# Optimization experiments

Measured on AMD Instinct MI355X. Metric: run time of the kernel, lower is better.

## Reference

```python
import jax, jax.numpy as jnp
import numpy as np

N_NODES = 50000
N_EDGES = 200000
D = 128
LN_EPS = 1e-5


def _layer_norm(x, g, b):
    mu = jnp.mean(x, axis=-1, keepdims=True)
    var = jnp.mean(jnp.square(x - mu), axis=-1, keepdims=True)
    return (x - mu) * jax.lax.rsqrt(var + LN_EPS) * g + b


def _mlp(x, W1, b1, W2, b2, W3, b3, g, beta):
    # 2 hidden ReLU layers + linear output + LayerNorm (MeshGraphNets style)
    h = jax.nn.relu(x @ W1 + b1)
    h = jax.nn.relu(h @ W2 + b2)
    h = h @ W3 + b3
    return _layer_norm(h, g, beta)


def setup_inputs() -> dict:
    key = jax.random.key(0)
    ks = jax.random.split(key, 12)
    d = {}
    d["node_features"] = jax.random.normal(ks[0], (N_NODES, D), dtype=jnp.float32)
    d["edge_features"] = jax.random.normal(ks[1], (N_EDGES, D), dtype=jnp.float32)
    d["senders"] = jax.random.randint(ks[2], (N_EDGES,), 0, N_NODES, dtype=jnp.int32)
    d["receivers"] = jax.random.randint(ks[3], (N_EDGES,), 0, N_NODES, dtype=jnp.int32)
    def lin(k, fan_in, fan_out):
        return jax.random.normal(k, (fan_in, fan_out), dtype=jnp.float32) / np.sqrt(fan_in)
    # edge MLP: [3D] -> D -> D -> D
    d["We1"] = lin(ks[4], 3 * D, D); d["be1"] = jnp.zeros((D,), jnp.float32)
    d["We2"] = lin(ks[5], D, D);     d["be2"] = jnp.zeros((D,), jnp.float32)
    d["We3"] = lin(ks[6], D, D);     d["be3"] = jnp.zeros((D,), jnp.float32)
    d["ge"] = jnp.ones((D,), jnp.float32); d["bege"] = jnp.zeros((D,), jnp.float32)
    # node MLP: [2D] -> D -> D -> D
    d["Wn1"] = lin(ks[7], 2 * D, D); d["bn1"] = jnp.zeros((D,), jnp.float32)
    d["Wn2"] = lin(ks[8], D, D);     d["bn2"] = jnp.zeros((D,), jnp.float32)
    d["Wn3"] = lin(ks[9], D, D);     d["bn3"] = jnp.zeros((D,), jnp.float32)
    d["gn"] = jnp.ones((D,), jnp.float32); d["begn"] = jnp.zeros((D,), jnp.float32)
    return d


def reference(node_features, edge_features, senders, receivers,
              We1, be1, We2, be2, We3, be3, ge, bege,
              Wn1, bn1, Wn2, bn2, Wn3, bn3, gn, begn):
    num_nodes = node_features.shape[0]
    # --- edge update: gather sender/receiver feats, concat, edge MLP ---
    edge_in = jnp.concatenate(
        [node_features[senders], node_features[receivers], edge_features], axis=-1)  # [E, 3D]
    new_edge = _mlp(edge_in, We1, be1, We2, be2, We3, be3, ge, bege)  # [E, D]
    # --- node update: scatter-sum aggregate, concat, node MLP ---
    agg = jax.ops.segment_sum(new_edge, receivers, num_segments=num_nodes)  # [N, D]
    node_in = jnp.concatenate([node_features, agg], axis=-1)  # [N, 2D]
    new_node = _mlp(node_in, Wn1, bn1, Wn2, bn2, Wn3, bn3, gn, begn)
    # --- residuals ---
    new_node = new_node + node_features
    new_edge = new_edge + edge_features
    return new_node, new_edge
```

## Files before the change

kernel.cpp:

```cpp
#include <hip/hip_runtime.h>

#define NNODES 50000
#define NEDGES 200000
#define DD 128
#define LN_EPS 1e-5f
#define NTH 256

typedef __attribute__((ext_vector_type(8))) short bf16x8;
typedef __attribute__((ext_vector_type(4))) float f32x4;

template<int N> struct ic { static constexpr int value = N; };

__device__ __forceinline__ unsigned short bf_rne(float f) {
    union { float f; unsigned u; } v; v.f = f;
    return (unsigned short)((v.u + 0x7fffu + ((v.u >> 16) & 1u)) >> 16);
}

__device__ __forceinline__ void gload_lds16(const void* g, void* l) {
    __builtin_amdgcn_global_load_lds(
        (const __attribute__((address_space(1))) void*)g,
        (__attribute__((address_space(3))) void*)l, 16, 0, 0);
}

__global__ void build_wimg(const float* __restrict__ We1, const float* __restrict__ We2,
                           const float* __restrict__ We3, const float* __restrict__ Wn1,
                           const float* __restrict__ Wn2, const float* __restrict__ Wn3,
                           char* __restrict__ img_e, char* __restrict__ img_n) {
    int tid = blockIdx.x * NTH + threadIdx.x;
    const float* W; char* dst; int q;
    if      (tid <  6144) { W = We1; dst = img_e;             q = tid;         }
    else if (tid <  8192) { W = We2; dst = img_e + 12 * 8192; q = tid - 6144;  }
    else if (tid < 10240) { W = We3; dst = img_e + 16 * 8192; q = tid - 8192;  }
    else if (tid < 14336) { W = Wn1; dst = img_n;             q = tid - 10240; }
    else if (tid < 16384) { W = Wn2; dst = img_n + 8 * 8192;  q = tid - 14336; }
    else if (tid < 18432) { W = Wn3; dst = img_n + 12 * 8192; q = tid - 16384; }
    else return;
    int c = q >> 9, rem = q & 511, n = rem >> 2, g = rem & 3;
    int S = ((g + (n >> 2)) & 3) ^ (n & 3);
    int k0 = c * 32 + g * 8;
    unsigned short o[8];
    #pragma unroll
    for (int e = 0; e < 8; ++e)
        o[e] = bf_rne(W[(size_t)(k0 + e) * DD + n]);
    uint4 val;
    val.x = (unsigned)o[0] | ((unsigned)o[1] << 16);
    val.y = (unsigned)o[2] | ((unsigned)o[3] << 16);
    val.z = (unsigned)o[4] | ((unsigned)o[5] << 16);
    val.w = (unsigned)o[6] | ((unsigned)o[7] << 16);
    *(uint4*)(dst + (size_t)c * 8192 + n * 64 + S * 16) = val;
}

__global__ void csr_histo(const int* __restrict__ recv, int* __restrict__ cnt) {
    int e = blockIdx.x * NTH + threadIdx.x;
    if (e < NEDGES) atomicAdd(&cnt[recv[e]], 1);
}

__global__ __launch_bounds__(1024)
void csr_scan(const int* __restrict__ cnt, int* __restrict__ off, int* __restrict__ cursor) {
    __shared__ int part[1024];
    const int t = threadIdx.x;
    const int CH = (NNODES + 1023) / 1024;
    const int base = t * CH;
    int s = 0;
    for (int i = 0; i < CH; ++i) {
        int idx = base + i;
        if (idx < NNODES) s += cnt[idx];
    }
    part[t] = s;
    __syncthreads();
    for (int d = 1; d < 1024; d <<= 1) {
        int v = (t >= d) ? part[t - d] : 0;
        __syncthreads();
        part[t] += v;
        __syncthreads();
    }
    int run = (t == 0) ? 0 : part[t - 1];
    for (int i = 0; i < CH; ++i) {
        int idx = base + i;
        if (idx < NNODES) {
            off[idx] = run; cursor[idx] = run;
            run += cnt[idx];
        }
    }
    if (t == 1023) off[NNODES] = NEDGES;
}

__global__ void csr_fill(const int* __restrict__ recv, int* __restrict__ cursor,
                         int* __restrict__ elist) {
    int e = blockIdx.x * NTH + threadIdx.x;
    if (e < NEDGES) {
        int p = atomicAdd(&cursor[recv[e]], 1);
        elist[p] = e;
    }
}

__global__ __launch_bounds__(NTH)
void aggregate(const float* __restrict__ oute, const float* __restrict__ edgef,
               const int* __restrict__ off, const int* __restrict__ elist,
               float* __restrict__ agg) {
    const int n = blockIdx.x * 4 + (threadIdx.x >> 6);
    const int l = threadIdx.x & 63;
    if (n >= NNODES) return;
    const int j0 = off[n], j1 = off[n + 1];
    float ax = 0.f, ay = 0.f, bx = 0.f, by = 0.f;
    int j = j0;
    for (; j + 1 < j1; j += 2) {
        const int e0 = elist[j], e1 = elist[j + 1];
        const float2 o0 = ((const float2*)(oute  + (size_t)e0 * DD))[l];
        const float2 f0 = ((const float2*)(edgef + (size_t)e0 * DD))[l];
        const float2 o1 = ((const float2*)(oute  + (size_t)e1 * DD))[l];
        const float2 f1 = ((const float2*)(edgef + (size_t)e1 * DD))[l];
        ax += o0.x - f0.x; ay += o0.y - f0.y;
        bx += o1.x - f1.x; by += o1.y - f1.y;
    }
    if (j < j1) {
        const int e = elist[j];
        const float2 o  = ((const float2*)(oute  + (size_t)e * DD))[l];
        const float2 ef = ((const float2*)(edgef + (size_t)e * DD))[l];
        ax += o.x - ef.x; ay += o.y - ef.y;
    }
    float2 r; r.x = ax + bx; r.y = ay + by;
    ((float2*)(agg + (size_t)n * DD))[l] = r;
}

template<int MODE>
__global__ __launch_bounds__(NTH, 3)
void mgn_mfma(const float* __restrict__ nodef, const float* __restrict__ edgef,
              const int* __restrict__ senders, const int* __restrict__ receivers,
              const char* __restrict__ img,
              const float* __restrict__ b1, const float* __restrict__ b2,
              const float* __restrict__ b3,
              const float* __restrict__ gamma, const float* __restrict__ beta,
              const float* __restrict__ agg, float* __restrict__ outp)
{
    __shared__ char Wbuf[4 * 8192];
    __shared__ char Hb[16384];

    const int t  = threadIdx.x;
    const int w  = t >> 6;
    const int l  = t & 63;
    const int lr = l & 15;
    const int g  = l >> 4;
    const int m_local = w * 16 + lr;
    const int row0 = blockIdx.x * 64;
    const int gm = row0 + m_local;
    constexpr int NROWS = (MODE == 0) ? NEDGES : NNODES;
    constexpr int NK1   = (MODE == 0) ? 12 : 8;
    constexpr int NCH   = NK1 + 8;
    const int gmc = gm < NROWS ? gm : NROWS - 1;
    const unsigned swz = (unsigned)(lr & 7) << 4;
    const int aoff = lr * 64 + ((((g + (lr >> 2)) & 3) ^ (lr & 3)) << 4);

    int srow = 0, rrow = 0;
    if (MODE == 0) { srow = senders[gmc]; rrow = receivers[gmc]; }

    f32x4 acc[8];
    const f32x4 fzero = {0.f, 0.f, 0.f, 0.f};
    #pragma unroll
    for (int nt = 0; nt < 8; ++nt) acc[nt] = fzero;

    f32x4 barr[3][2];

    auto stageW = [&](int c) {
        const char* src = img + (size_t)c * 8192 + w * 1024 + l * 16;
        char* dstl = Wbuf + (c & 3) * 8192 + w * 1024;
        gload_lds16(src, dstl);
        gload_lds16(src + 4096, dstl + 4096);
    };

    auto loadBG = [&](int c, f32x4* dst) {
        const float* base;
        if (MODE == 0) {
            base = (c < 4) ? nodef + (size_t)srow * DD
                 : (c < 8) ? nodef + (size_t)rrow * DD
                           : edgef + (size_t)gmc * DD;
        } else {
            base = (c < 4) ? nodef + (size_t)gmc * DD
                           : agg   + (size_t)gmc * DD;
        }
        const float* p = base + (c & 3) * 32 + g * 8;
        dst[0] = *(const f32x4*)p;
        dst[1] = *(const f32x4*)(p + 4);
    };

    auto cvtB = [&](const f32x4* br) {
        bf16x8 r;
        #pragma unroll
        for (int i = 0; i < 4; ++i) r[i]     = (short)bf_rne(br[0][i]);
        #pragma unroll
        for (int i = 0; i < 4; ++i) r[4 + i] = (short)bf_rne(br[1][i]);
        return r;
    };

    auto loadBH = [&](int ks) {
        const char* p = &Hb[(ks >> 1) * 8192] + m_local * 128
                      + ((unsigned)((ks & 1) * 64 + g * 16) ^ swz);
        return *(const bf16x8*)p;
    };

    auto epiH = [&](const float* bias) {
        #pragma unroll
        for (int nt = 0; nt < 8; ++nt) {
            f32x4 bv = *(const f32x4*)(bias + nt * 16 + g * 4);
            unsigned short h[4];
            #pragma unroll
            for (int r = 0; r < 4; ++r)
                h[r] = bf_rne(fmaxf(acc[nt][r] + bv[r], 0.f));
            char* p = &Hb[(nt >> 2) * 8192] + m_local * 128
                    + ((unsigned)(((nt & 3) * 2 + (g >> 1)) * 16) ^ swz) + (g & 1) * 8;
            unsigned lo = (unsigned)h[0] | ((unsigned)h[1] << 16);
            unsigned hi = (unsigned)h[2] | ((unsigned)h[3] << 16);
            *(unsigned long long*)p = (unsigned long long)lo | ((unsigned long long)hi << 32);
            acc[nt] = fzero;
        }
    };

    auto compute = [&](auto cc) {
        constexpr int c = decltype(cc)::value;
        const char* bp = Wbuf + (c & 3) * 8192 + aoff;
        bf16x8 a[8];
        #pragma unroll
        for (int nt = 0; nt < 8; ++nt)
            a[nt] = *(const bf16x8*)(bp + nt * 1024);
        bf16x8 b;
        if constexpr (c < NK1) b = cvtB(barr[c % 3]);
        else                   b = loadBH((c - NK1) & 3);
        #pragma unroll
        for (int nt = 0; nt < 8; ++nt)
            acc[nt] = __builtin_amdgcn_mfma_f32_16x16x32_bf16(a[nt], b, acc[nt], 0, 0, 0);
    };

#define PITER(C, VM)                                                        \
    {                                                                       \
        if constexpr ((C) + 2 < NCH) stageW((C) + 2);                       \
        __builtin_amdgcn_sched_barrier(0);                                  \
        if constexpr ((C) + 2 < NK1) loadBG((C) + 2, barr[((C) + 2) % 3]);  \
        __builtin_amdgcn_sched_barrier(0);                                  \
        asm volatile("s_waitcnt vmcnt(" #VM ")" ::: "memory");              \
        __builtin_amdgcn_sched_barrier(0);                                  \
        __builtin_amdgcn_s_barrier();                                       \
        __builtin_amdgcn_sched_barrier(0);                                  \
        compute(ic<(C)>{});                                                 \
    }

    stageW(0);
    __builtin_amdgcn_sched_barrier(0);
    loadBG(0, barr[0]);
    __builtin_amdgcn_sched_barrier(0);
    stageW(1);
    __builtin_amdgcn_sched_barrier(0);
    loadBG(1, barr[1]);
    __builtin_amdgcn_sched_barrier(0);

    if constexpr (MODE == 0) {
        PITER(0, 8)  PITER(1, 8)  PITER(2, 8)  PITER(3, 8)  PITER(4, 8)
        PITER(5, 8)  PITER(6, 8)  PITER(7, 8)  PITER(8, 8)  PITER(9, 8)
        PITER(10, 6) PITER(11, 4)
        epiH(b1);
        PITER(12, 4) PITER(13, 4) PITER(14, 4) PITER(15, 4)
        epiH(b2);
        PITER(16, 4) PITER(17, 4) PITER(18, 2) PITER(19, 0)
    } else {
        PITER(0, 8)  PITER(1, 8)  PITER(2, 8)  PITER(3, 8)  PITER(4, 8)
        PITER(5, 8)  PITER(6, 6)  PITER(7, 4)
        epiH(b1);
        PITER(8, 4)  PITER(9, 4)  PITER(10, 4) PITER(11, 4)
        epiH(b2);
        PITER(12, 4) PITER(13, 4) PITER(14, 2) PITER(15, 0)
    }
#undef PITER

    float vsum = 0.f, vsq = 0.f;
    #pragma unroll
    for (int nt = 0; nt < 8; ++nt) {
        f32x4 bv = *(const f32x4*)(b3 + nt * 16 + g * 4);
        #pragma unroll
        for (int r = 0; r < 4; ++r) {
            float v = acc[nt][r] + bv[r];
            acc[nt][r] = v;
            vsum += v; vsq += v * v;
        }
    }
    vsum += __shfl_xor(vsum, 16); vsum += __shfl_xor(vsum, 32);
    vsq  += __shfl_xor(vsq, 16);  vsq  += __shfl_xor(vsq, 32);
    const float mu = vsum * (1.f / DD);
    const float rs = rsqrtf(vsq * (1.f / DD) - mu * mu + LN_EPS);

    if (gm < NROWS) {
        const float* resid = ((MODE == 0) ? edgef : nodef) + (size_t)gm * DD;
        #pragma unroll
        for (int nt = 0; nt < 8; ++nt) {
            const int n0 = nt * 16 + g * 4;
            f32x4 gv = *(const f32x4*)(gamma + n0);
            f32x4 bv = *(const f32x4*)(beta + n0);
            f32x4 rv = *(const f32x4*)(resid + n0);
            f32x4 o;
            #pragma unroll
            for (int r = 0; r < 4; ++r)
                o[r] = (acc[nt][r] - mu) * rs * gv[r] + bv[r] + rv[r];
            *(f32x4*)(outp + (size_t)gm * DD + n0) = o;
        }
    }
}

extern "C" void kernel_launch(void* const* d_in, const int* in_sizes, int n_in,
                              void* d_out, int out_size, void* d_ws, size_t ws_size,
                              hipStream_t stream) {
    const float* nodef = (const float*)d_in[0];
    const float* edgef = (const float*)d_in[1];
    const int* senders   = (const int*)d_in[2];
    const int* receivers = (const int*)d_in[3];
    const float* We1 = (const float*)d_in[4],  *be1 = (const float*)d_in[5];
    const float* We2 = (const float*)d_in[6],  *be2 = (const float*)d_in[7];
    const float* We3 = (const float*)d_in[8],  *be3 = (const float*)d_in[9];
    const float* ge  = (const float*)d_in[10], *bege = (const float*)d_in[11];
    const float* Wn1 = (const float*)d_in[12], *bn1 = (const float*)d_in[13];
    const float* Wn2 = (const float*)d_in[14], *bn2 = (const float*)d_in[15];
    const float* Wn3 = (const float*)d_in[16], *bn3 = (const float*)d_in[17];
    const float* gn  = (const float*)d_in[18], *begn = (const float*)d_in[19];

    float* out_node = (float*)d_out;
    float* out_edge = (float*)d_out + (size_t)NNODES * DD;

    char* ws = (char*)d_ws;
    size_t o = 0;
    float* agg  = (float*)(ws + o); o += (size_t)NNODES * DD * 4;
    char* img_e = ws + o;           o += 20 * 8192;
    char* img_n = ws + o;           o += 16 * 8192;
    int* cnt    = (int*)(ws + o);   o += NNODES * 4;
    int* cursor = (int*)(ws + o);   o += NNODES * 4;
    int* off    = (int*)(ws + o);   o += (NNODES + 4) * 4;
    int* elist  = (int*)(ws + o);   o += NEDGES * 4;

    hipMemsetAsync(cnt, 0, NNODES * 4, stream);
    build_wimg<<<72, NTH, 0, stream>>>(We1, We2, We3, Wn1, Wn2, Wn3, img_e, img_n);

    const int egrid = (NEDGES + NTH - 1) / NTH;
    csr_histo<<<egrid, NTH, 0, stream>>>(receivers, cnt);
    csr_scan<<<1, 1024, 0, stream>>>(cnt, off, cursor);
    csr_fill<<<egrid, NTH, 0, stream>>>(receivers, cursor, elist);

    mgn_mfma<0><<<dim3((NEDGES + 63) / 64), dim3(NTH), 0, stream>>>(
        nodef, edgef, senders, receivers, img_e,
        be1, be2, be3, ge, bege, agg, out_edge);

    aggregate<<<(NNODES + 3) / 4, NTH, 0, stream>>>(out_edge, edgef, off, elist, agg);

    mgn_mfma<1><<<dim3((NNODES + 63) / 64), dim3(NTH), 0, stream>>>(
        nodef, edgef, senders, receivers, img_n,
        bn1, bn2, bn3, gn, begn, agg, out_node);
}
```

Baseline: 324.3 us.

## Switch fused MLP kernel to 32x32x16 MFMA tiles with 128-row blocks

The fused MLP kernel moves from 16x16x32 bf16 MFMA to 32x32x16 MFMA, so each wave now covers 32 rows and a block covers 128 rows. The weight image layout and LDS swizzles are rebuilt to match the new operand fragments. Weight staging goes from a 4-slot to a 5-slot ring with a prefetch distance of 3 chunks. The hidden-activation buffer doubles and launch bounds drop to 2 blocks per CU. The aim is higher MFMA throughput and more weight reuse per LDS load, at the cost of more registers and LDS and lower occupancy.

Result: no change. 329.2 us (+1.5%).

```diff
diff --git a/kernel.cpp b/kernel.cpp
--- a/kernel.cpp
+++ b/kernel.cpp
@@ -8,6 +8,7 @@
 
 typedef __attribute__((ext_vector_type(8))) short bf16x8;
 typedef __attribute__((ext_vector_type(4))) float f32x4;
+typedef __attribute__((ext_vector_type(16))) float f32x16;
 
 template<int N> struct ic { static constexpr int value = N; };
 
@@ -35,9 +36,11 @@
     else if (tid < 16384) { W = Wn2; dst = img_n + 8 * 8192;  q = tid - 14336; }
     else if (tid < 18432) { W = Wn3; dst = img_n + 12 * 8192; q = tid - 16384; }
     else return;
-    int c = q >> 9, rem = q & 511, n = rem >> 2, g = rem & 3;
-    int S = ((g + (n >> 2)) & 3) ^ (n & 3);
-    int k0 = c * 32 + g * 8;
+    int c = q >> 9, rem = q & 511;
+    int ntile = rem >> 7, r2 = rem & 127, n32 = r2 >> 2, ks = r2 & 3;
+    int n = ntile * 32 + n32;
+    int sx = (n32 + (n32 >> 2)) & 3;
+    int k0 = c * 32 + ks * 8;
     unsigned short o[8];
     #pragma unroll
     for (int e = 0; e < 8; ++e)
@@ -47,7 +50,7 @@
     val.y = (unsigned)o[2] | ((unsigned)o[3] << 16);
     val.z = (unsigned)o[4] | ((unsigned)o[5] << 16);
     val.w = (unsigned)o[6] | ((unsigned)o[7] << 16);
-    *(uint4*)(dst + (size_t)c * 8192 + n * 64 + S * 16) = val;
+    *(uint4*)(dst + (size_t)c * 8192 + ntile * 2048 + n32 * 64 + ((ks ^ sx) << 4)) = val;
 }
 
 __global__ void csr_histo(const int* __restrict__ recv, int* __restrict__ cnt) {
@@ -124,7 +127,7 @@
 }
 
 template<int MODE>
-__global__ __launch_bounds__(NTH, 3)
+__global__ __launch_bounds__(NTH, 2)
 void mgn_mfma(const float* __restrict__ nodef, const float* __restrict__ edgef,
               const int* __restrict__ senders, const int* __restrict__ receivers,
               const char* __restrict__ img,
@@ -133,37 +136,37 @@
               const float* __restrict__ gamma, const float* __restrict__ beta,
               const float* __restrict__ agg, float* __restrict__ outp)
 {
-    __shared__ char Wbuf[4 * 8192];
-    __shared__ char Hb[16384];
+    __shared__ char Wbuf[5 * 8192];
+    __shared__ char Hb[4 * 8192];
 
     const int t  = threadIdx.x;
     const int w  = t >> 6;
     const int l  = t & 63;
-    const int lr = l & 15;
-    const int g  = l >> 4;
-    const int m_local = w * 16 + lr;
-    const int row0 = blockIdx.x * 64;
-    const int gm = row0 + m_local;
+    const int ln = l & 31;
+    const int hi = l >> 5;
+    const int row0 = blockIdx.x * 128;
+    const int gm = row0 + w * 32 + ln;
     constexpr int NROWS = (MODE == 0) ? NEDGES : NNODES;
     constexpr int NK1   = (MODE == 0) ? 12 : 8;
     constexpr int NCH   = NK1 + 8;
     const int gmc = gm < NROWS ? gm : NROWS - 1;
-    const unsigned swz = (unsigned)(lr & 7) << 4;
-    const int aoff = lr * 64 + ((((g + (lr >> 2)) & 3) ^ (lr & 3)) << 4);
+    const int sxA = (ln + (ln >> 2)) & 3;
+    const int sxH = ln & 15;
 
     int srow = 0, rrow = 0;
     if (MODE == 0) { srow = senders[gmc]; rrow = receivers[gmc]; }
 
-    f32x4 acc[8];
-    const f32x4 fzero = {0.f, 0.f, 0.f, 0.f};
+    const f32x16 fz = {0.f,0.f,0.f,0.f,0.f,0.f,0.f,0.f,
+                       0.f,0.f,0.f,0.f,0.f,0.f,0.f,0.f};
+    f32x16 acc[4];
     #pragma unroll
-    for (int nt = 0; nt < 8; ++nt) acc[nt] = fzero;
-
-    f32x4 barr[3][2];
+    for (int nt = 0; nt < 4; ++nt) acc[nt] = fz;
+
+    f32x4 barr[3][4];
 
     auto stageW = [&](int c) {
-        const char* src = img + (size_t)c * 8192 + w * 1024 + l * 16;
-        char* dstl = Wbuf + (c & 3) * 8192 + w * 1024;
+        const char* src = img + (size_t)c * 8192 + t * 16;
+        char* dstl = Wbuf + (c % 5) * 8192 + t * 16;
         gload_lds16(src, dstl);
         gload_lds16(src + 4096, dstl + 4096);
     };
@@ -178,9 +181,11 @@
             base = (c < 4) ? nodef + (size_t)gmc * DD
                            : agg   + (size_t)gmc * DD;
         }
-        const float* p = base + (c & 3) * 32 + g * 8;
+        const float* p = base + (c & 3) * 32 + hi * 8;
         dst[0] = *(const f32x4*)p;
         dst[1] = *(const f32x4*)(p + 4);
+        dst[2] = *(const f32x4*)(p + 16);
+        dst[3] = *(const f32x4*)(p + 20);
     };
 
     auto cvtB = [&](const f32x4* br) {
@@ -192,47 +197,53 @@
         return r;
     };
 
-    auto loadBH = [&](int ks) {
-        const char* p = &Hb[(ks >> 1) * 8192] + m_local * 128
-                      + ((unsigned)((ks & 1) * 64 + g * 16) ^ swz);
+    auto loadBH = [&](int ks, int kh) {
+        const char* p = Hb + w * 8192 + ln * 256
+                      + (((ks * 4 + kh * 2 + hi) ^ sxH) << 4);
         return *(const bf16x8*)p;
     };
 
     auto epiH = [&](const float* bias) {
         #pragma unroll
-        for (int nt = 0; nt < 8; ++nt) {
-            f32x4 bv = *(const f32x4*)(bias + nt * 16 + g * 4);
-            unsigned short h[4];
+        for (int nt = 0; nt < 4; ++nt) {
             #pragma unroll
-            for (int r = 0; r < 4; ++r)
-                h[r] = bf_rne(fmaxf(acc[nt][r] + bv[r], 0.f));
-            char* p = &Hb[(nt >> 2) * 8192] + m_local * 128
-                    + ((unsigned)(((nt & 3) * 2 + (g >> 1)) * 16) ^ swz) + (g & 1) * 8;
-            unsigned lo = (unsigned)h[0] | ((unsigned)h[1] << 16);
-            unsigned hi = (unsigned)h[2] | ((unsigned)h[3] << 16);
-            *(unsigned long long*)p = (unsigned long long)lo | ((unsigned long long)hi << 32);
-            acc[nt] = fzero;
+            for (int rq = 0; rq < 4; ++rq) {
+                f32x4 bv = *(const f32x4*)(bias + nt * 32 + rq * 8 + hi * 4);
+                unsigned short h[4];
+                #pragma unroll
+                for (int j = 0; j < 4; ++j)
+                    h[j] = bf_rne(fmaxf(acc[nt][rq * 4 + j] + bv[j], 0.f));
+                char* p = Hb + w * 8192 + ln * 256
+                        + (((nt * 4 + rq) ^ sxH) << 4) + hi * 8;
+                unsigned lo = (unsigned)h[0] | ((unsigned)h[1] << 16);
+                unsigned hx = (unsigned)h[2] | ((unsigned)h[3] << 16);
+                *(unsigned long long*)p =
+                    (unsigned long long)lo | ((unsigned long long)hx << 32);
+            }
+            acc[nt] = fz;
         }
     };
 
     auto compute = [&](auto cc) {
         constexpr int c = decltype(cc)::value;
-        const char* bp = Wbuf + (c & 3) * 8192 + aoff;
-        bf16x8 a[8];
-        #pragma unroll
-        for (int nt = 0; nt < 8; ++nt)
-            a[nt] = *(const bf16x8*)(bp + nt * 1024);
-        bf16x8 b;
-        if constexpr (c < NK1) b = cvtB(barr[c % 3]);
-        else                   b = loadBH((c - NK1) & 3);
-        #pragma unroll
-        for (int nt = 0; nt < 8; ++nt)
-            acc[nt] = __builtin_amdgcn_mfma_f32_16x16x32_bf16(a[nt], b, acc[nt], 0, 0, 0);
+        const char* bp = Wbuf + (c % 5) * 8192 + ln * 64;
+        #pragma unroll
+        for (int kh = 0; kh < 2; ++kh) {
+            bf16x8 b;
+            if constexpr (c < NK1) b = cvtB(&barr[c % 3][kh * 2]);
+            else                   b = loadBH((c - NK1) & 3, kh);
+            #pragma unroll
+            for (int nt = 0; nt < 4; ++nt) {
+                bf16x8 a = *(const bf16x8*)(bp + nt * 2048
+                            + (((kh * 2 + hi) ^ sxA) << 4));
+                acc[nt] = __builtin_amdgcn_mfma_f32_32x32x16_bf16(a, b, acc[nt], 0, 0, 0);
+            }
+        }
     };
 
 #define PITER(C, VM)                                                        \
     {                                                                       \
-        if constexpr ((C) + 2 < NCH) stageW((C) + 2);                       \
+        if constexpr ((C) + 3 < NCH) stageW((C) + 3);                       \
         __builtin_amdgcn_sched_barrier(0);                                  \
         if constexpr ((C) + 2 < NK1) loadBG((C) + 2, barr[((C) + 2) % 3]);  \
         __builtin_amdgcn_sched_barrier(0);                                  \
@@ -251,54 +262,62 @@
     __builtin_amdgcn_sched_barrier(0);
     loadBG(1, barr[1]);
     __builtin_amdgcn_sched_barrier(0);
+    stageW(2);
+    __builtin_amdgcn_sched_barrier(0);
 
     if constexpr (MODE == 0) {
-        PITER(0, 8)  PITER(1, 8)  PITER(2, 8)  PITER(3, 8)  PITER(4, 8)
-        PITER(5, 8)  PITER(6, 8)  PITER(7, 8)  PITER(8, 8)  PITER(9, 8)
-        PITER(10, 6) PITER(11, 4)
+        PITER(0, 18)  PITER(1, 18)  PITER(2, 18)  PITER(3, 22)  PITER(4, 22)
+        PITER(5, 22)  PITER(6, 22)  PITER(7, 22)  PITER(8, 22)  PITER(9, 22)
+        PITER(10, 18) PITER(11, 14)
         epiH(b1);
-        PITER(12, 4) PITER(13, 4) PITER(14, 4) PITER(15, 4)
+        PITER(12, 10) PITER(13, 6)  PITER(14, 6)  PITER(15, 6)
         epiH(b2);
-        PITER(16, 4) PITER(17, 4) PITER(18, 2) PITER(19, 0)
+        PITER(16, 6)  PITER(17, 4)  PITER(18, 2)  PITER(19, 0)
     } else {
-        PITER(0, 8)  PITER(1, 8)  PITER(2, 8)  PITER(3, 8)  PITER(4, 8)
-        PITER(5, 8)  PITER(6, 6)  PITER(7, 4)
+        PITER(0, 18)  PITER(1, 18)  PITER(2, 18)  PITER(3, 22)  PITER(4, 22)
+        PITER(5, 22)  PITER(6, 18)  PITER(7, 14)
         epiH(b1);
-        PITER(8, 4)  PITER(9, 4)  PITER(10, 4) PITER(11, 4)
+        PITER(8, 10)  PITER(9, 6)   PITER(10, 6)  PITER(11, 6)
         epiH(b2);
-        PITER(12, 4) PITER(13, 4) PITER(14, 2) PITER(15, 0)
+        PITER(12, 6)  PITER(13, 4)  PITER(14, 2)  PITER(15, 0)
     }
 #undef PITER
 
     float vsum = 0.f, vsq = 0.f;
     #pragma unroll
-    for (int nt = 0; nt < 8; ++nt) {
-        f32x4 bv = *(const f32x4*)(b3 + nt * 16 + g * 4);
-        #pragma unroll
-        for (int r = 0; r < 4; ++r) {
-            float v = acc[nt][r] + bv[r];
-            acc[nt][r] = v;
-            vsum += v; vsq += v * v;
-        }
-    }
-    vsum += __shfl_xor(vsum, 16); vsum += __shfl_xor(vsum, 32);
-    vsq  += __shfl_xor(vsq, 16);  vsq  += __shfl_xor(vsq, 32);
+    for (int nt = 0; nt < 4; ++nt) {
+        #pragma unroll
+        for (int rq = 0; rq < 4; ++rq) {
+            f32x4 bv = *(const f32x4*)(b3 + nt * 32 + rq * 8 + hi * 4);
+            #pragma unroll
+            for (int j = 0; j < 4; ++j) {
+                float v = acc[nt][rq * 4 + j] + bv[j];
+                acc[nt][rq * 4 + j] = v;
+                vsum += v; vsq += v * v;
+            }
+        }
+    }
+    vsum += __shfl_xor(vsum, 32);
+    vsq  += __shfl_xor(vsq, 32);
     const float mu = vsum * (1.f / DD);
     const float rs = rsqrtf(vsq * (1.f / DD) - mu * mu + LN_EPS);
 
     if (gm < NROWS) {
         const float* resid = ((MODE == 0) ? edgef : nodef) + (size_t)gm * DD;
         #pragma unroll
-        for (int nt = 0; nt < 8; ++nt) {
-            const int n0 = nt * 16 + g * 4;
-            f32x4 gv = *(const f32x4*)(gamma + n0);
-            f32x4 bv = *(const f32x4*)(beta + n0);
-            f32x4 rv = *(const f32x4*)(resid + n0);
-            f32x4 o;
+        for (int nt = 0; nt < 4; ++nt) {
             #pragma unroll
-            for (int r = 0; r < 4; ++r)
-                o[r] = (acc[nt][r] - mu) * rs * gv[r] + bv[r] + rv[r];
-            *(f32x4*)(outp + (size_t)gm * DD + n0) = o;
+            for (int rq = 0; rq < 4; ++rq) {
+                const int n0 = nt * 32 + rq * 8 + hi * 4;
+                f32x4 gv = *(const f32x4*)(gamma + n0);
+                f32x4 bv = *(const f32x4*)(beta + n0);
+                f32x4 rv = *(const f32x4*)(resid + n0);
+                f32x4 o;
+                #pragma unroll
+                for (int j = 0; j < 4; ++j)
+                    o[j] = (acc[nt][rq * 4 + j] - mu) * rs * gv[j] + bv[j] + rv[j];
+                *(f32x4*)(outp + (size_t)gm * DD + n0) = o;
+            }
         }
     }
 }
@@ -340,13 +359,13 @@
     csr_scan<<<1, 1024, 0, stream>>>(cnt, off, cursor);
     csr_fill<<<egrid, NTH, 0, stream>>>(receivers, cursor, elist);
 
-    mgn_mfma<0><<<dim3((NEDGES + 63) / 64), dim3(NTH), 0, stream>>>(
+    mgn_mfma<0><<<dim3((NEDGES + 127) / 128), dim3(NTH), 0, stream>>>(
         nodef, edgef, senders, receivers, img_e,
         be1, be2, be3, ge, bege, agg, out_edge);
 
     aggregate<<<(NNODES + 3) / 4, NTH, 0, stream>>>(out_edge, edgef, off, elist, agg);
 
-    mgn_mfma<1><<<dim3((NNODES + 63) / 64), dim3(NTH), 0, stream>>>(
+    mgn_mfma<1><<<dim3((NNODES + 127) / 128), dim3(NTH), 0, stream>>>(
         nodef, edgef, senders, receivers, img_n,
         bn1, bn2, bn3, gn, begn, agg, out_node);
 }
```
